# Optimization experiments

Hardware: AMD Instinct MI355X
Metric: run time of the kernel (lower is better)

The kernel has to match this reference:

```python
import jax, jax.numpy as jnp
import numpy as np

N = 100_000   # nodes
E = 640_000   # edges
H = 128       # hidden_dim
L = 4         # num_layers
C = 2         # num_classes
G = 128       # graphs in batch

def setup_inputs() -> dict:
    key = jax.random.key(0)
    ks = jax.random.split(key, 8)
    x = jax.random.randint(ks[0], (N, 1), 0, 2)
    edge_index = jax.random.randint(ks[1], (2, E), 0, N)
    batch = jnp.sort(jax.random.randint(ks[2], (N,), 0, G))
    embed = jax.random.normal(ks[3], (2, H), jnp.float32)
    Ws = jax.random.normal(ks[4], (L, H, H), jnp.float32) * (1.0 / np.sqrt(H))
    bs = jnp.zeros((L, H), jnp.float32)
    W_out = jax.random.normal(ks[5], (H, C), jnp.float32) * (1.0 / np.sqrt(H))
    b_out = jnp.zeros((C,), jnp.float32)
    return dict(x=x, edge_index=edge_index, batch=batch, embed=embed,
                Ws=Ws, bs=bs, W_out=W_out, b_out=b_out)

def reference(x, edge_index, batch, embed, Ws, bs, W_out, b_out):
    src, dst = edge_index[0], edge_index[1]
    # symmetric GCN normalization with self-loops (PyG GCNConv default)
    deg = jax.ops.segment_sum(jnp.ones(E, jnp.float32), dst, num_segments=N) + 1.0
    dinv = jax.lax.rsqrt(deg)
    enorm = (dinv[src] * dinv[dst])[:, None]   # per-edge norm
    snorm = (dinv * dinv)[:, None]             # self-loop norm

    h = embed[x[:, 0]]                          # [N, H] embedding lookup
    n_layers = Ws.shape[0]
    for l in range(n_layers):
        t = h @ Ws[l]                           # linear transform [N, H]
        agg = jax.ops.segment_sum(t[src] * enorm, dst, num_segments=N) \
              + t * snorm + bs[l]
        h = jax.nn.relu(agg) if l < n_layers - 1 else agg

    # global mean pool over graph ids
    counts = jax.ops.segment_sum(jnp.ones(N, jnp.float32), batch, num_segments=G)
    pooled = jax.ops.segment_sum(h, batch, num_segments=G) \
             / jnp.maximum(counts, 1.0)[:, None]   # [G, H]
    return pooled @ W_out + b_out                  # [G, C]
```

## Files before the change

kernel.cpp:

```cpp
#include <hip/hip_runtime.h>

typedef __attribute__((ext_vector_type(8))) short bf16x8;
typedef __attribute__((ext_vector_type(4))) float f32x4;
typedef __attribute__((ext_vector_type(2))) float f32x2;

__device__ inline unsigned short bf16_rtn(float f) {
  unsigned u = __float_as_uint(f);
  unsigned r = u + 0x7fffu + ((u >> 16) & 1u);
  return (unsigned short)(r >> 16);
}

__device__ inline void split_bf16(float f, unsigned short& hi, unsigned short& lo) {
  hi = bf16_rtn(f);
  float fh = __uint_as_float((unsigned)hi << 16);
  lo = bf16_rtn(f - fh);
}

__device__ inline float bf16_to_f(unsigned short v) {
  return __uint_as_float((unsigned)v << 16);
}

__device__ inline unsigned char f_to_fp8(float f) {
  int r = __builtin_amdgcn_cvt_pk_fp8_f32(f, f, 0, false);
  return (unsigned char)(r & 0xff);
}
__device__ inline f32x2 fp8x2_to_f(unsigned short v) {
  return __builtin_amdgcn_cvt_pk_f32_fp8((int)v, false);
}

__global__ void k_init(int* __restrict__ deg, int* __restrict__ gpz, int N, int M,
                       const float* __restrict__ Ws, const float* __restrict__ embed,
                       unsigned short* __restrict__ wphi,
                       unsigned short* __restrict__ wplo,
                       float* __restrict__ T,
                       unsigned char* __restrict__ t_a,
                       unsigned char* __restrict__ t_b) {
  int i = blockIdx.x * 256 + threadIdx.x;
  if (i < N) deg[i] = 0;
  if (i < M) gpz[i] = 0;
  int l = blockIdx.x;
  if (l < 3) {
    const float* W = Ws + (size_t)(l + 1) * 128 * 128;
    unsigned short* dh = wphi + (size_t)l * 16384;
    unsigned short* dl = wplo + (size_t)l * 16384;
    for (int idx = threadIdx.x; idx < 16384; idx += 256) {
      int j = idx & 7;
      int lane = (idx >> 3) & 63;
      int c = (idx >> 9) & 3;
      int ct = idx >> 11;
      int k = c * 32 + ((lane >> 4) * 8) + j;
      int n = ct * 16 + (lane & 15);
      unsigned short hi, lo;
      split_bf16(W[k * 128 + n], hi, lo);
      dh[idx] = hi;
      dl[idx] = lo;
    }
  } else if (l == 3) {
    int t = threadIdx.x;
    int r = t >> 7, c = t & 127;
    float acc = 0.f;
    for (int k = 0; k < 128; ++k)
      acc += embed[r * 128 + k] * Ws[k * 128 + c];
    T[r * 128 + c] = acc;
  } else if (l == 4) {
    int t = threadIdx.x;
    if (t < 32)      ((unsigned*)(t_a + (size_t)N * 128))[t] = 0u;
    else if (t < 64) ((unsigned*)(t_b + (size_t)N * 128))[t - 32] = 0u;
  }
}


__global__ void k_hist(const int* __restrict__ dst, int* __restrict__ deg,
                       int* __restrict__ posr, int E) {
  int e = blockIdx.x * 256 + threadIdx.x;
  if (e < E) posr[e] = atomicAdd(&deg[dst[e]], 1);
}

__global__ void k_scan1(const int* __restrict__ deg, int* __restrict__ rowptr,
                        int* __restrict__ bsum, float* __restrict__ dpk,
                        const int* __restrict__ x, const int* __restrict__ batch,
                        int* __restrict__ gstart, int* __restrict__ gend, int N) {
  __shared__ int s[256];
  int t = threadIdx.x;
  int i = blockIdx.x * 256 + t;
  int v = (i < N) ? deg[i] : 0;
  if (i < N) {
    float di = rsqrtf((float)v + 1.0f);
    dpk[i] = x[i] ? -di : di;
    int g = batch[i];
    if (i == 0 || batch[i - 1] != g) gstart[g] = i;
    if (i == N - 1 || batch[i + 1] != g) gend[g] = i + 1;
  }
  s[t] = v;
  __syncthreads();
  for (int off = 1; off < 256; off <<= 1) {
    int u = (t >= off) ? s[t - off] : 0;
    __syncthreads();
    s[t] += u;
    __syncthreads();
  }
  if (i < N) rowptr[i] = s[t] - v;
  if (t == 255) bsum[blockIdx.x] = s[255];
}

__global__ void k_scan2(const int* __restrict__ bsum, int* __restrict__ boff, int nb) {
  __shared__ int s[512];
  int t = threadIdx.x;
  int v = (t < nb) ? bsum[t] : 0;
  s[t] = v;
  __syncthreads();
  for (int off = 1; off < 512; off <<= 1) {
    int u = (t >= off) ? s[t - off] : 0;
    __syncthreads();
    s[t] += u;
    __syncthreads();
  }
  boff[t] = s[t] - v;
}

__global__ void k_scan3(int* __restrict__ rowptr, const int* __restrict__ boff,
                        int N, int E) {
  int i = blockIdx.x * 256 + threadIdx.x;
  if (i < N) rowptr[i] += boff[i >> 8];
  if (i == 0) rowptr[N] = E;
}

__global__ void k_scatter(const int* __restrict__ src, const int* __restrict__ dst,
                          const int* __restrict__ posr, const int* __restrict__ rowptr,
                          const float* __restrict__ dpk,
                          int2* __restrict__ epack, int E) {
  int e = blockIdx.x * 256 + threadIdx.x;
  if (e >= E) return;
  int s = src[e], d = dst[e];
  int pos = rowptr[d] + posr[e];
  epack[pos] = make_int2(s, __float_as_int(dpk[s]));
}


__device__ inline void acc16(float* a, uint4 p) {
  f32x2 v;
  v = __builtin_amdgcn_cvt_pk_f32_fp8((int)p.x, false); a[0]  += v.x; a[1]  += v.y;
  v = __builtin_amdgcn_cvt_pk_f32_fp8((int)p.x, true);  a[2]  += v.x; a[3]  += v.y;
  v = __builtin_amdgcn_cvt_pk_f32_fp8((int)p.y, false); a[4]  += v.x; a[5]  += v.y;
  v = __builtin_amdgcn_cvt_pk_f32_fp8((int)p.y, true);  a[6]  += v.x; a[7]  += v.y;
  v = __builtin_amdgcn_cvt_pk_f32_fp8((int)p.z, false); a[8]  += v.x; a[9]  += v.y;
  v = __builtin_amdgcn_cvt_pk_f32_fp8((int)p.z, true);  a[10] += v.x; a[11] += v.y;
  v = __builtin_amdgcn_cvt_pk_f32_fp8((int)p.w, false); a[12] += v.x; a[13] += v.y;
  v = __builtin_amdgcn_cvt_pk_f32_fp8((int)p.w, true);  a[14] += v.x; a[15] += v.y;
}

__device__ inline void gather8(const unsigned char* __restrict__ tin,
                               const int2* __restrict__ epack,
                               int r0, int deg, int l8, int N,
                               float* a) {
  int dcap = deg < 16 ? deg : 16;
  int slo = N, shi = N;
  if (2 * l8 < dcap)     slo = epack[r0 + 2 * l8].x;
  if (2 * l8 + 1 < dcap) shi = epack[r0 + 2 * l8 + 1].x;

  uint4 p[16];
  #pragma unroll
  for (int k = 0; k < 8; ++k) {
    int se = __shfl(slo, k, 8);
    int so = __shfl(shi, k, 8);
    p[2 * k]     = *(const uint4*)(tin + (size_t)((unsigned)se * 128u + ((unsigned)l8 << 4)));
    p[2 * k + 1] = *(const uint4*)(tin + (size_t)((unsigned)so * 128u + ((unsigned)l8 << 4)));
  }
  #pragma unroll
  for (int k = 0; k < 16; ++k) acc16(a, p[k]);

  if (__builtin_expect(deg > 16, 0)) {
    for (int e = r0 + 16; e < r0 + deg; ++e) {
      int s = epack[e].x;
      uint4 q = *(const uint4*)(tin + (size_t)((unsigned)s * 128u + ((unsigned)l8 << 4)));
      acc16(a, q);
    }
  }
}

__global__ __launch_bounds__(256)
void k_agg_gemm(const unsigned char* __restrict__ tin,
                const int* __restrict__ rowptr,
                const int2* __restrict__ epack,
                const float* __restrict__ dpk, const float* __restrict__ bvec,
                const unsigned short* __restrict__ wphi,
                const unsigned short* __restrict__ wplo,
                unsigned char* __restrict__ tout, int N) {
  __shared__ unsigned short hT[32 * 136];
  int lane = threadIdx.x & 63;
  int wave = threadIdx.x >> 6;
  int g8 = lane >> 3, l8 = lane & 7;
  int nloc = wave * 8 + g8;
  int i0 = blockIdx.x * 32;
  int i = i0 + nloc;

  unsigned u[8];
  if (i < N) {
    int r0 = rowptr[i], r1 = rowptr[i + 1];
    uint4 ps = *(const uint4*)(tin + (size_t)i * 128 + (l8 << 4));
    float dp = dpk[i];

    float a[16];
    #pragma unroll
    for (int k = 0; k < 16; ++k) a[k] = 0.f;
    gather8(tin, epack, r0, r1 - r0, l8, N, a);
    acc16(a, ps);

    float di = fabsf(dp);
    const float4* bp = (const float4*)(bvec + 16 * l8);
    float4 b0 = bp[0], b1 = bp[1], b2 = bp[2], b3 = bp[3];
    float bb[16] = {b0.x, b0.y, b0.z, b0.w, b1.x, b1.y, b1.z, b1.w,
                    b2.x, b2.y, b2.z, b2.w, b3.x, b3.y, b3.z, b3.w};
    #pragma unroll
    for (int k = 0; k < 8; ++k) {
      float v0 = fmaxf(di * a[2 * k]     + bb[2 * k],     0.f);
      float v1 = fmaxf(di * a[2 * k + 1] + bb[2 * k + 1], 0.f);
      u[k] = (unsigned)bf16_rtn(v0) | ((unsigned)bf16_rtn(v1) << 16);
    }
  } else {
    #pragma unroll
    for (int k = 0; k < 8; ++k) u[k] = 0u;
  }
  {
    uint4* hp = (uint4*)&hT[nloc * 136 + 16 * l8];
    hp[0] = make_uint4(u[0], u[1], u[2], u[3]);
    hp[1] = make_uint4(u[4], u[5], u[6], u[7]);
  }
  __syncthreads();

  int q = lane >> 4;
  int m = lane & 15;
  const bf16x8* bh_base = (const bf16x8*)wphi;
  const bf16x8* bl_base = (const bf16x8*)wplo;

  f32x4 acc[2][2];
  #pragma unroll
  for (int tt = 0; tt < 2; ++tt)
    #pragma unroll
    for (int ctl = 0; ctl < 2; ++ctl)
      acc[tt][ctl] = (f32x4){0.f, 0.f, 0.f, 0.f};

  #pragma unroll
  for (int c = 0; c < 4; ++c) {
    bf16x8 a0 = *(const bf16x8*)(hT + m * 136 + c * 32 + q * 8);
    bf16x8 a1 = *(const bf16x8*)(hT + (16 + m) * 136 + c * 32 + q * 8);
    #pragma unroll
    for (int ctl = 0; ctl < 2; ++ctl) {
      int ct = wave * 2 + ctl;
      bf16x8 bh = bh_base[(ct * 4 + c) * 64 + lane];
      bf16x8 bl = bl_base[(ct * 4 + c) * 64 + lane];
      acc[0][ctl] = __builtin_amdgcn_mfma_f32_16x16x32_bf16(a0, bh, acc[0][ctl], 0, 0, 0);
      acc[0][ctl] = __builtin_amdgcn_mfma_f32_16x16x32_bf16(a0, bl, acc[0][ctl], 0, 0, 0);
      acc[1][ctl] = __builtin_amdgcn_mfma_f32_16x16x32_bf16(a1, bh, acc[1][ctl], 0, 0, 0);
      acc[1][ctl] = __builtin_amdgcn_mfma_f32_16x16x32_bf16(a1, bl, acc[1][ctl], 0, 0, 0);
    }
  }

  #pragma unroll
  for (int tt = 0; tt < 2; ++tt)
    #pragma unroll
    for (int ctl = 0; ctl < 2; ++ctl) {
      int ct = wave * 2 + ctl;
      #pragma unroll
      for (int r = 0; r < 4; ++r) {
        int row = i0 + tt * 16 + q * 4 + r;
        if (row < N) {
          float sc = fabsf(dpk[row]);
          tout[(size_t)row * 128 + ct * 16 + m] = f_to_fp8(sc * acc[tt][ctl][r]);
        }
      }
    }
}

__global__ __launch_bounds__(256)
void k_agg_pool(const unsigned char* __restrict__ tin,
                const int* __restrict__ rowptr,
                const int2* __restrict__ epack,
                const float* __restrict__ dpk, const float* __restrict__ bvec,
                const int* __restrict__ batch,
                float* __restrict__ pooled, int N) {
  __shared__ float sh[32][128];
  __shared__ int sg[32];
  int lane = threadIdx.x & 63;
  int g8 = lane >> 3, l8 = lane & 7;
  int nloc = (threadIdx.x >> 6) * 8 + g8;
  int i = blockIdx.x * 32 + nloc;
  if (threadIdx.x < 32) sg[threadIdx.x] = -1;
  __syncthreads();
  if (i < N) {
    int r0 = rowptr[i], r1 = rowptr[i + 1];
    uint4 ps = *(const uint4*)(tin + (size_t)i * 128 + (l8 << 4));
    float dp = dpk[i];

    float a[16];
    #pragma unroll
    for (int k = 0; k < 16; ++k) a[k] = 0.f;
    gather8(tin, epack, r0, r1 - r0, l8, N, a);
    acc16(a, ps);

    float di = fabsf(dp);
    const float4* bp = (const float4*)(bvec + 16 * l8);
    float4 b0 = bp[0], b1 = bp[1], b2 = bp[2], b3 = bp[3];
    float bb[16] = {b0.x, b0.y, b0.z, b0.w, b1.x, b1.y, b1.z, b1.w,
                    b2.x, b2.y, b2.z, b2.w, b3.x, b3.y, b3.z, b3.w};
    #pragma unroll
    for (int k = 0; k < 16; ++k)
      sh[nloc][16 * l8 + k] = di * a[k] + bb[k];
    if (l8 == 0) sg[nloc] = batch[i];
  }
  __syncthreads();
  if (threadIdx.x < 128) {
    int c = threadIdx.x;
    float acc = 0.f;
    int cur = sg[0];
    #pragma unroll
    for (int w2 = 0; w2 < 32; ++w2) {
      int gw = sg[w2];
      if (gw < 0) break;
      if (gw != cur) {
        atomicAdd(&pooled[cur * 128 + c], acc);
        acc = 0.f;
        cur = gw;
      }
      acc += sh[w2][c];
    }
    atomicAdd(&pooled[cur * 128 + c], acc);
  }
}

__device__ inline void gemm_tile8(const unsigned short* hT,
                                  const unsigned short* __restrict__ wphi,
                                  const unsigned short* __restrict__ wplo,
                                  const float* __restrict__ dpk,
                                  unsigned char* __restrict__ tout, int i0, int N) {
  int ct = threadIdx.x >> 6;
  int lane = threadIdx.x & 63;
  int q = lane >> 4;
  int m = lane & 15;
  const bf16x8* bh_base = (const bf16x8*)wphi;
  const bf16x8* bl_base = (const bf16x8*)wplo;

  f32x4 acc0 = (f32x4){0.f, 0.f, 0.f, 0.f};
  f32x4 acc1 = (f32x4){0.f, 0.f, 0.f, 0.f};

  #pragma unroll
  for (int c = 0; c < 4; ++c) {
    bf16x8 a0 = *(const bf16x8*)(hT + (m) * 136 + c * 32 + q * 8);
    bf16x8 a1 = *(const bf16x8*)(hT + (16 + m) * 136 + c * 32 + q * 8);
    bf16x8 bh = bh_base[(ct * 4 + c) * 64 + lane];
    bf16x8 bl = bl_base[(ct * 4 + c) * 64 + lane];
    acc0 = __builtin_amdgcn_mfma_f32_16x16x32_bf16(a0, bh, acc0, 0, 0, 0);
    acc0 = __builtin_amdgcn_mfma_f32_16x16x32_bf16(a0, bl, acc0, 0, 0, 0);
    acc1 = __builtin_amdgcn_mfma_f32_16x16x32_bf16(a1, bh, acc1, 0, 0, 0);
    acc1 = __builtin_amdgcn_mfma_f32_16x16x32_bf16(a1, bl, acc1, 0, 0, 0);
  }

  #pragma unroll
  for (int r = 0; r < 4; ++r) {
    int row0 = i0 + q * 4 + r;
    int row1 = row0 + 16;
    if (row0 < N) {
      float sc = fabsf(dpk[row0]);
      tout[(size_t)row0 * 128 + ct * 16 + m] = f_to_fp8(sc * acc0[r]);
    }
    if (row1 < N) {
      float sc = fabsf(dpk[row1]);
      tout[(size_t)row1 * 128 + ct * 16 + m] = f_to_fp8(sc * acc1[r]);
    }
  }
}

__global__ __launch_bounds__(512)
void k_l1_gemm(const int* __restrict__ rowptr,
               const int2* __restrict__ epack,
               const float* __restrict__ dpk, const float* __restrict__ T,
               const float* __restrict__ b0,
               const unsigned short* __restrict__ wphi,
               const unsigned short* __restrict__ wplo,
               unsigned char* __restrict__ tout, int N) {
  __shared__ unsigned short hT[32 * 136];
  int wave = threadIdx.x >> 6;
  int lane = threadIdx.x & 63;
  int i0 = blockIdx.x * 32;

  for (int j = wave * 4; j < wave * 4 + 4; ++j) {
    int i = i0 + j;
    if (i >= N) break;
    int r0 = rowptr[i], r1 = rowptr[i + 1];
    float sabs = 0.f, sneg = 0.f;
    for (int e = r0 + lane; e < r1; e += 64) {
      float wv = __int_as_float(epack[e].y);
      float aw = fabsf(wv);
      sabs += aw;
      if (wv < 0.f) sneg += aw;
    }
    for (int mm = 32; mm >= 1; mm >>= 1) {
      sabs += __shfl_xor(sabs, mm, 64);
      sneg += __shfl_xor(sneg, mm, 64);
    }
    float dp = dpk[i];
    float di = fabsf(dp);
    float sn = di * di;
    float c1 = di * sneg;
    float c0 = di * (sabs - sneg);
    if (dp < 0.f) c1 += sn; else c0 += sn;
    float v0 = fmaxf(c0 * T[2 * lane]     + c1 * T[128 + 2 * lane]     + b0[2 * lane],     0.f);
    float v1 = fmaxf(c0 * T[2 * lane + 1] + c1 * T[128 + 2 * lane + 1] + b0[2 * lane + 1], 0.f);
    *(unsigned*)&hT[j * 136 + 2 * lane] = (unsigned)bf16_rtn(v0) | ((unsigned)bf16_rtn(v1) << 16);
  }
  __syncthreads();
  gemm_tile8(hT, wphi, wplo, dpk, tout, i0, N);
}

__global__ void k_out(const float* __restrict__ pooled, const int* __restrict__ gstart,
                      const int* __restrict__ gend, const float* __restrict__ W_out,
                      const float* __restrict__ b_out, float* __restrict__ out, int G) {
  __shared__ float sp[128];
  int g = blockIdx.x;
  int j = threadIdx.x;
  float cnt = (float)(gend[g] - gstart[g]);
  sp[j] = pooled[g * 128 + j] / fmaxf(cnt, 1.f);
  __syncthreads();
  if (j < 2) {
    float o = b_out[j];
    for (int k = 0; k < 128; ++k)
      o += sp[k] * W_out[k * 2 + j];
    out[g * 2 + j] = o;
  }
}

extern "C" void kernel_launch(void* const* d_in, const int* in_sizes, int n_in,
                              void* d_out, int out_size, void* d_ws, size_t ws_size,
                              hipStream_t stream) {
  const int*   x     = (const int*)d_in[0];
  const int*   ei    = (const int*)d_in[1];
  const int*   batch = (const int*)d_in[2];
  const float* embed = (const float*)d_in[3];
  const float* Ws    = (const float*)d_in[4];
  const float* bs    = (const float*)d_in[5];
  const float* W_out = (const float*)d_in[6];
  const float* b_out = (const float*)d_in[7];
  float* out = (float*)d_out;

  int N = in_sizes[2];
  int E = in_sizes[1] / 2;
  int G = out_size / 2;

  const int* src = ei;
  const int* dst = ei + E;

  char* w = (char*)d_ws;
  auto alloc = [&](size_t bytes) {
    char* p = w;
    w += (bytes + 255) & ~(size_t)255;
    return p;
  };
  int*   deg    = (int*)  alloc((size_t)N * 4);
  float* dpk    = (float*)alloc((size_t)N * 4);
  int*   rowptr = (int*)  alloc((size_t)(N + 1) * 4);
  int*   posr   = (int*)  alloc((size_t)E * 4);
  int*   bsum   = (int*)  alloc(512 * 4);
  int*   boff   = (int*)  alloc(512 * 4);
  int*   gstart = (int*)  alloc((size_t)G * 4);
  int*   gend   = (int*)  alloc((size_t)G * 4);
  float* pooled = (float*)alloc((size_t)G * 128 * 4);
  float* T      = (float*)alloc(256 * 4);
  unsigned short* wphi = (unsigned short*)alloc((size_t)3 * 16384 * 2);
  unsigned short* wplo = (unsigned short*)alloc((size_t)3 * 16384 * 2);
  int2*  epack  = (int2*) alloc((size_t)E * 8);
  unsigned char* t_a = (unsigned char*)alloc((size_t)(N + 1) * 128);
  unsigned char* t_b = (unsigned char*)alloc((size_t)(N + 1) * 128);

  int nbN = (N + 255) / 256;
  int nbE = (E + 255) / 256;
  int ntile = (N + 31) / 32;
  int nagg = (N + 31) / 32;
  int M = G * 130;

  k_init<<<nbN, 256, 0, stream>>>(deg, gstart, N, M, Ws, embed, wphi, wplo, T, t_a, t_b);
  k_hist<<<nbE, 256, 0, stream>>>(dst, deg, posr, E);
  k_scan1<<<nbN, 256, 0, stream>>>(deg, rowptr, bsum, dpk, x, batch, gstart, gend, N);
  k_scan2<<<1, 512, 0, stream>>>(bsum, boff, nbN);
  k_scan3<<<nbN, 256, 0, stream>>>(rowptr, boff, N, E);
  k_scatter<<<nbE, 256, 0, stream>>>(src, dst, posr, rowptr, dpk, epack, E);

  k_l1_gemm<<<ntile, 512, 0, stream>>>(rowptr, epack, dpk, T, bs,
                                       wphi, wplo, t_a, N);
  k_agg_gemm<<<nagg, 256, 0, stream>>>(t_a, rowptr, epack, dpk, bs + 128,
                                       wphi + 16384, wplo + 16384, t_b, N);
  k_agg_gemm<<<nagg, 256, 0, stream>>>(t_b, rowptr, epack, dpk, bs + 256,
                                       wphi + 32768, wplo + 32768, t_a, N);
  k_agg_pool<<<nagg, 256, 0, stream>>>(t_a, rowptr, epack, dpk, bs + 384,
                                       batch, pooled, N);
  k_out<<<G, 128, 0, stream>>>(pooled, gstart, gend, W_out, b_out, out, G);
}
```

Before: 292.8 us.

## Drop posr via atomic row heads, add compact esrc array, shrink pool blocks

The CSR build no longer stores a per-edge position from the histogram pass. The scatter pass takes slots with atomics on a per-row head array, and two scan kernels are merged into one that reduces the block sums directly. The scatter also writes a separate 4-byte source index array, so the aggregation gathers read half the bytes they read from the 8-byte epack. Other changes: the unrolled gather prefetch drops from 16 to 12 neighbours to ease register pressure, and the pooling kernel uses 64-thread blocks of 8 nodes. In exchange the edge order within each row becomes nondeterministic, the scatter pays atomic contention, and there is an extra array write.

```diff
diff --git a/kernel.cpp b/kernel.cpp
--- a/kernel.cpp
+++ b/kernel.cpp
@@ -16,16 +16,9 @@
   lo = bf16_rtn(f - fh);
 }
 
-__device__ inline float bf16_to_f(unsigned short v) {
-  return __uint_as_float((unsigned)v << 16);
-}
-
 __device__ inline unsigned char f_to_fp8(float f) {
   int r = __builtin_amdgcn_cvt_pk_fp8_f32(f, f, 0, false);
   return (unsigned char)(r & 0xff);
-}
-__device__ inline f32x2 fp8x2_to_f(unsigned short v) {
-  return __builtin_amdgcn_cvt_pk_f32_fp8((int)v, false);
 }
 
 __global__ void k_init(int* __restrict__ deg, int* __restrict__ gpz, int N, int M,
@@ -70,10 +63,9 @@
 }
 
 
-__global__ void k_hist(const int* __restrict__ dst, int* __restrict__ deg,
-                       int* __restrict__ posr, int E) {
+__global__ void k_hist(const int* __restrict__ dst, int* __restrict__ deg, int E) {
   int e = blockIdx.x * 256 + threadIdx.x;
-  if (e < E) posr[e] = atomicAdd(&deg[dst[e]], 1);
+  if (e < E) atomicAdd(&deg[dst[e]], 1);
 }
 
 __global__ void k_scan1(const int* __restrict__ deg, int* __restrict__ rowptr,
@@ -103,37 +95,38 @@
   if (t == 255) bsum[blockIdx.x] = s[255];
 }
 
-__global__ void k_scan2(const int* __restrict__ bsum, int* __restrict__ boff, int nb) {
-  __shared__ int s[512];
-  int t = threadIdx.x;
-  int v = (t < nb) ? bsum[t] : 0;
-  s[t] = v;
-  __syncthreads();
-  for (int off = 1; off < 512; off <<= 1) {
-    int u = (t >= off) ? s[t - off] : 0;
+__global__ void k_scanB(int* __restrict__ rowptr, int* __restrict__ rowhead,
+                        const int* __restrict__ bsum, int N, int E) {
+  __shared__ int red[256];
+  int b = blockIdx.x, t = threadIdx.x;
+  int s = 0;
+  for (int j = t; j < b; j += 256) s += bsum[j];
+  red[t] = s;
+  __syncthreads();
+  for (int off = 128; off >= 1; off >>= 1) {
+    if (t < off) red[t] += red[t + off];
     __syncthreads();
-    s[t] += u;
-    __syncthreads();
-  }
-  boff[t] = s[t] - v;
-}
-
-__global__ void k_scan3(int* __restrict__ rowptr, const int* __restrict__ boff,
-                        int N, int E) {
-  int i = blockIdx.x * 256 + threadIdx.x;
-  if (i < N) rowptr[i] += boff[i >> 8];
+  }
+  int boff = red[0];
+  int i = b * 256 + t;
+  if (i < N) {
+    int v = rowptr[i] + boff;
+    rowptr[i] = v;
+    rowhead[i] = v;
+  }
   if (i == 0) rowptr[N] = E;
 }
 
 __global__ void k_scatter(const int* __restrict__ src, const int* __restrict__ dst,
-                          const int* __restrict__ posr, const int* __restrict__ rowptr,
+                          int* __restrict__ rowhead,
                           const float* __restrict__ dpk,
-                          int2* __restrict__ epack, int E) {
+                          int2* __restrict__ epack, int* __restrict__ esrc, int E) {
   int e = blockIdx.x * 256 + threadIdx.x;
   if (e >= E) return;
   int s = src[e], d = dst[e];
-  int pos = rowptr[d] + posr[e];
+  int pos = atomicAdd(&rowhead[d], 1);
   epack[pos] = make_int2(s, __float_as_int(dpk[s]));
+  esrc[pos] = s;
 }
 
 
@@ -150,28 +143,28 @@
 }
 
 __device__ inline void gather8(const unsigned char* __restrict__ tin,
-                               const int2* __restrict__ epack,
+                               const int* __restrict__ esrc,
                                int r0, int deg, int l8, int N,
                                float* a) {
-  int dcap = deg < 16 ? deg : 16;
+  int dcap = deg < 12 ? deg : 12;
   int slo = N, shi = N;
-  if (2 * l8 < dcap)     slo = epack[r0 + 2 * l8].x;
-  if (2 * l8 + 1 < dcap) shi = epack[r0 + 2 * l8 + 1].x;
-
-  uint4 p[16];
-  #pragma unroll
-  for (int k = 0; k < 8; ++k) {
+  if (2 * l8 < dcap)     slo = esrc[r0 + 2 * l8];
+  if (2 * l8 + 1 < dcap) shi = esrc[r0 + 2 * l8 + 1];
+
+  uint4 p[12];
+  #pragma unroll
+  for (int k = 0; k < 6; ++k) {
     int se = __shfl(slo, k, 8);
     int so = __shfl(shi, k, 8);
     p[2 * k]     = *(const uint4*)(tin + (size_t)((unsigned)se * 128u + ((unsigned)l8 << 4)));
     p[2 * k + 1] = *(const uint4*)(tin + (size_t)((unsigned)so * 128u + ((unsigned)l8 << 4)));
   }
   #pragma unroll
-  for (int k = 0; k < 16; ++k) acc16(a, p[k]);
-
-  if (__builtin_expect(deg > 16, 0)) {
-    for (int e = r0 + 16; e < r0 + deg; ++e) {
-      int s = epack[e].x;
+  for (int k = 0; k < 12; ++k) acc16(a, p[k]);
+
+  if (__builtin_expect(deg > 12, 0)) {
+    for (int e = r0 + 12; e < r0 + deg; ++e) {
+      int s = esrc[e];
       uint4 q = *(const uint4*)(tin + (size_t)((unsigned)s * 128u + ((unsigned)l8 << 4)));
       acc16(a, q);
     }
@@ -181,7 +174,7 @@
 __global__ __launch_bounds__(256)
 void k_agg_gemm(const unsigned char* __restrict__ tin,
                 const int* __restrict__ rowptr,
-                const int2* __restrict__ epack,
+                const int* __restrict__ esrc,
                 const float* __restrict__ dpk, const float* __restrict__ bvec,
                 const unsigned short* __restrict__ wphi,
                 const unsigned short* __restrict__ wplo,
@@ -203,7 +196,7 @@
     float a[16];
     #pragma unroll
     for (int k = 0; k < 16; ++k) a[k] = 0.f;
-    gather8(tin, epack, r0, r1 - r0, l8, N, a);
+    gather8(tin, esrc, r0, r1 - r0, l8, N, a);
     acc16(a, ps);
 
     float di = fabsf(dp);
@@ -272,20 +265,19 @@
     }
 }
 
-__global__ __launch_bounds__(256)
+__global__ __launch_bounds__(64)
 void k_agg_pool(const unsigned char* __restrict__ tin,
                 const int* __restrict__ rowptr,
-                const int2* __restrict__ epack,
+                const int* __restrict__ esrc,
                 const float* __restrict__ dpk, const float* __restrict__ bvec,
                 const int* __restrict__ batch,
                 float* __restrict__ pooled, int N) {
-  __shared__ float sh[32][128];
-  __shared__ int sg[32];
-  int lane = threadIdx.x & 63;
+  __shared__ float sh[8][128];
+  __shared__ int sg[8];
+  int lane = threadIdx.x;
   int g8 = lane >> 3, l8 = lane & 7;
-  int nloc = (threadIdx.x >> 6) * 8 + g8;
-  int i = blockIdx.x * 32 + nloc;
-  if (threadIdx.x < 32) sg[threadIdx.x] = -1;
+  int i = blockIdx.x * 8 + g8;
+  if (lane < 8) sg[lane] = -1;
   __syncthreads();
   if (i < N) {
     int r0 = rowptr[i], r1 = rowptr[i + 1];
@@ -295,7 +287,7 @@
     float a[16];
     #pragma unroll
     for (int k = 0; k < 16; ++k) a[k] = 0.f;
-    gather8(tin, epack, r0, r1 - r0, l8, N, a);
+    gather8(tin, esrc, r0, r1 - r0, l8, N, a);
     acc16(a, ps);
 
     float di = fabsf(dp);
@@ -305,16 +297,17 @@
                     b2.x, b2.y, b2.z, b2.w, b3.x, b3.y, b3.z, b3.w};
     #pragma unroll
     for (int k = 0; k < 16; ++k)
-      sh[nloc][16 * l8 + k] = di * a[k] + bb[k];
-    if (l8 == 0) sg[nloc] = batch[i];
-  }
-  __syncthreads();
-  if (threadIdx.x < 128) {
-    int c = threadIdx.x;
+      sh[g8][16 * l8 + k] = di * a[k] + bb[k];
+    if (l8 == 0) sg[g8] = batch[i];
+  }
+  __syncthreads();
+  #pragma unroll
+  for (int cc = 0; cc < 2; ++cc) {
+    int c = threadIdx.x + 64 * cc;
     float acc = 0.f;
     int cur = sg[0];
     #pragma unroll
-    for (int w2 = 0; w2 < 32; ++w2) {
+    for (int w2 = 0; w2 < 8; ++w2) {
       int gw = sg[w2];
       if (gw < 0) break;
       if (gw != cur) {
@@ -324,7 +317,7 @@
       }
       acc += sh[w2][c];
     }
-    atomicAdd(&pooled[cur * 128 + c], acc);
+    if (cur >= 0) atomicAdd(&pooled[cur * 128 + c], acc);
   }
 }
 
@@ -458,9 +451,8 @@
   int*   deg    = (int*)  alloc((size_t)N * 4);
   float* dpk    = (float*)alloc((size_t)N * 4);
   int*   rowptr = (int*)  alloc((size_t)(N + 1) * 4);
-  int*   posr   = (int*)  alloc((size_t)E * 4);
+  int*   rowhead= (int*)  alloc((size_t)N * 4);
   int*   bsum   = (int*)  alloc(512 * 4);
-  int*   boff   = (int*)  alloc(512 * 4);
   int*   gstart = (int*)  alloc((size_t)G * 4);
   int*   gend   = (int*)  alloc((size_t)G * 4);
   float* pooled = (float*)alloc((size_t)G * 128 * 4);
@@ -468,29 +460,29 @@
   unsigned short* wphi = (unsigned short*)alloc((size_t)3 * 16384 * 2);
   unsigned short* wplo = (unsigned short*)alloc((size_t)3 * 16384 * 2);
   int2*  epack  = (int2*) alloc((size_t)E * 8);
+  int*   esrc   = (int*)  alloc((size_t)E * 4);
   unsigned char* t_a = (unsigned char*)alloc((size_t)(N + 1) * 128);
   unsigned char* t_b = (unsigned char*)alloc((size_t)(N + 1) * 128);
 
   int nbN = (N + 255) / 256;
   int nbE = (E + 255) / 256;
   int ntile = (N + 31) / 32;
-  int nagg = (N + 31) / 32;
+  int nagg = (N + 7) / 8;
   int M = G * 130;
 
   k_init<<<nbN, 256, 0, stream>>>(deg, gstart, N, M, Ws, embed, wphi, wplo, T, t_a, t_b);
-  k_hist<<<nbE, 256, 0, stream>>>(dst, deg, posr, E);
+  k_hist<<<nbE, 256, 0, stream>>>(dst, deg, E);
   k_scan1<<<nbN, 256, 0, stream>>>(deg, rowptr, bsum, dpk, x, batch, gstart, gend, N);
-  k_scan2<<<1, 512, 0, stream>>>(bsum, boff, nbN);
-  k_scan3<<<nbN, 256, 0, stream>>>(rowptr, boff, N, E);
-  k_scatter<<<nbE, 256, 0, stream>>>(src, dst, posr, rowptr, dpk, epack, E);
+  k_scanB<<<nbN, 256, 0, stream>>>(rowptr, rowhead, bsum, N, E);
+  k_scatter<<<nbE, 256, 0, stream>>>(src, dst, rowhead, dpk, epack, esrc, E);
 
   k_l1_gemm<<<ntile, 512, 0, stream>>>(rowptr, epack, dpk, T, bs,
                                        wphi, wplo, t_a, N);
-  k_agg_gemm<<<nagg, 256, 0, stream>>>(t_a, rowptr, epack, dpk, bs + 128,
-                                       wphi + 16384, wplo + 16384, t_b, N);
-  k_agg_gemm<<<nagg, 256, 0, stream>>>(t_b, rowptr, epack, dpk, bs + 256,
-                                       wphi + 32768, wplo + 32768, t_a, N);
-  k_agg_pool<<<nagg, 256, 0, stream>>>(t_a, rowptr, epack, dpk, bs + 384,
-                                       batch, pooled, N);
+  k_agg_gemm<<<ntile, 256, 0, stream>>>(t_a, rowptr, esrc, dpk, bs + 128,
+                                        wphi + 16384, wplo + 16384, t_b, N);
+  k_agg_gemm<<<ntile, 256, 0, stream>>>(t_b, rowptr, esrc, dpk, bs + 256,
+                                        wphi + 32768, wplo + 32768, t_a, N);
+  k_agg_pool<<<nagg, 64, 0, stream>>>(t_a, rowptr, esrc, dpk, bs + 384,
+                                      batch, pooled, N);
   k_out<<<G, 128, 0, stream>>>(pooled, gstart, gend, W_out, b_out, out, G);
 }
```

Result: slower. 309.2 us (+5.6%).
